# Kernel optimization log

Hardware: AMD Instinct MI355X
Metric: run time of the kernel (lower is better)

Reference implementation:

```python
import jax, jax.numpy as jnp
import numpy as np

HID = 64   # RNN_HID_SIZE
FEAT = 9   # feature dim, hard-coded in module
T = 36     # SEQ_LEN


def setup_inputs() -> dict:
    key = jax.random.key(0)
    ks = jax.random.split(key, 20)
    B = 16384

    def u(k, shape, stdv):
        return jax.random.uniform(k, shape, jnp.float32, -stdv, stdv)

    s_h = 1.0 / np.sqrt(HID)    # stdv for layers with 64 rows / fan-in 64
    s_f = 1.0 / np.sqrt(FEAT)   # stdv 1/3 for feature-sized layers
    s_c = 1.0 / np.sqrt(2 * FEAT)  # weight_combine: Linear(18, 9)

    inp = {
        "values": jax.random.normal(ks[0], (B, T, FEAT), jnp.float32),
        "masks": (jax.random.uniform(ks[1], (B, T, FEAT)) < 0.8).astype(jnp.float32),
        "deltas": jax.random.uniform(ks[2], (B, T, FEAT), jnp.float32, 0.0, 5.0),
        # TemporalDecay h: W [64, 9], stdv = 1/sqrt(64)
        "W_gh": u(ks[3], (HID, FEAT), s_h), "b_gh": u(ks[4], (HID,), s_h),
        # TemporalDecay x (diag): W [9, 9], stdv = 1/sqrt(9)
        "W_gx": u(ks[5], (FEAT, FEAT), s_f), "b_gx": u(ks[6], (FEAT,), s_f),
        # hist_reg: Linear(64, 9)
        "W_hist": u(ks[7], (FEAT, HID), s_h), "b_hist": u(ks[8], (FEAT,), s_h),
        "W_feat": u(ks[9], (FEAT, FEAT), s_f), "b_feat": u(ks[10], (FEAT,), s_f),
        # weight_combine: Linear(18, 9)
        "W_comb": u(ks[11], (FEAT, 2 * FEAT), s_c), "b_comb": u(ks[12], (FEAT,), s_c),
        # LSTMCell(18, 64): gates order i, f, g, o
        "W_ih": u(ks[13], (4 * HID, 2 * FEAT), s_h), "W_hh": u(ks[14], (4 * HID, HID), s_h),
        "b_ih": u(ks[15], (4 * HID,), s_h), "b_hh": u(ks[16], (4 * HID,), s_h),
    }
    return inp


def reference(values, masks, deltas, W_gh, b_gh, W_gx, b_gx, W_hist, b_hist,
              W_feat, b_feat, W_comb, b_comb, W_ih, W_hh, b_ih, b_hh):
    B = values.shape[0]
    dt = values.dtype
    eye = jnp.eye(FEAT, dtype=dt)
    Wgx_diag = W_gx * eye            # TemporalDecay diag mask
    Wfeat_off = W_feat * (1.0 - eye)

    # time-major for scan: [T, B, F]
    xs = (jnp.swapaxes(values, 0, 1), jnp.swapaxes(masks, 0, 1), jnp.swapaxes(deltas, 0, 1))

    def step(carry, xt):
        h, c, loss = carry
        x, m, d = xt
        gamma_h = jnp.exp(-jax.nn.relu(d @ W_gh.T + b_gh))   # [B, 64]
        gamma_x = jnp.exp(-jax.nn.relu(d @ Wgx_diag.T + b_gx))  # [B, 9]
        h = h * gamma_h
        x_h = h @ W_hist.T + b_hist
        denom = jnp.sum(m) + 1e-5
        x_c = m * x + (1.0 - m) * x_h
        z_h = x_c @ Wfeat_off.T + b_feat
        alpha = jnp.concatenate([gamma_x, m], axis=1) @ W_comb.T + b_comb
        c_h = alpha * z_h + (1.0 - alpha) * x_h
        loss = loss + (jnp.sum(jnp.abs(x - x_h) * m)
                       + jnp.sum(jnp.abs(x - z_h) * m)
                       + jnp.sum(jnp.abs(x - c_h) * m)) / denom
        c_c = m * x + (1.0 - m) * c_h
        inp = jnp.concatenate([c_c, m], axis=1)              # [B, 18]
        gates = inp @ W_ih.T + b_ih + h @ W_hh.T + b_hh      # [B, 256]
        i, f, g, o = jnp.split(gates, 4, axis=1)
        c = jax.nn.sigmoid(f) * c + jax.nn.sigmoid(i) * jnp.tanh(g)
        h = jax.nn.sigmoid(o) * jnp.tanh(c)
        return (h, c, loss), c_c

    init = (jnp.zeros((B, HID), dt), jnp.zeros((B, HID), dt), jnp.zeros((), dt))
    (_, _, loss), imps = jax.lax.scan(step, init, xs)
    imputations = jnp.swapaxes(imps, 0, 1)  # [B, T, F]
    return loss / T, imputations
```

## Files before the change

### kernel.cpp

```cpp
#include <hip/hip_runtime.h>

typedef _Float16 hh;
typedef _Float16 h2  __attribute__((ext_vector_type(2)));
typedef _Float16 v4h __attribute__((ext_vector_type(4)));
typedef _Float16 v8h __attribute__((ext_vector_type(8)));
typedef float v4f    __attribute__((ext_vector_type(4)));
typedef unsigned short u16;

#define T_STEPS 36
#define FEAT 9
#define HID 64
#define BT 32
#define SIN_STR 264
#define PK_STR 40

__device__ __forceinline__ float fast_exp2(float x) {
#if __has_builtin(__builtin_amdgcn_exp2f)
  return __builtin_amdgcn_exp2f(x);
#else
  return exp2f(x);
#endif
}
__device__ __forceinline__ float fast_rcp(float x) {
#if __has_builtin(__builtin_amdgcn_rcpf)
  return __builtin_amdgcn_rcpf(x);
#else
  return 1.f / x;
#endif
}
__device__ __forceinline__ float sigmoid_fast(float x) {
  return fast_rcp(1.f + fast_exp2(x * -1.442695041f));
}
__device__ __forceinline__ float tanh_fast(float x) {
  return 1.f - 2.f * fast_rcp(1.f + fast_exp2(x * 2.885390082f));
}
__device__ __forceinline__ float fdot2(h2 a, h2 b, float c) {
#if __has_builtin(__builtin_amdgcn_fdot2)
  return __builtin_amdgcn_fdot2(a, b, c, false);
#else
  return c + (float)a[0] * (float)b[0] + (float)a[1] * (float)b[1];
#endif
}
__device__ __forceinline__ h2 mkh2(hh a, hh b) { h2 r; r[0] = a; r[1] = b; return r; }
__device__ __forceinline__ v4f mfma16(v8h a, v8h b, v4f c) {
  return __builtin_amdgcn_mfma_f32_16x16x32_f16(a, b, c, 0, 0, 0);
}

__global__ void zero_ws(float* __restrict__ ws, float* __restrict__ out) {
  int tid = threadIdx.x;
  if (tid < T_STEPS) ws[tid] = 0.f;
  if (tid == 0) out[0] = 0.f;
}

__global__ __launch_bounds__(256) void denom_kernel(const float* __restrict__ masks,
                                                    float* __restrict__ ws) {
  __shared__ float red[T_STEPS];
  const int tid = threadIdx.x;
  if (tid < T_STEPS) red[tid] = 0.f;
  __syncthreads();
  const int idx = blockIdx.x * 256 + tid;
  const int t0 = (idx % 9) * 4;
  const float4* p = (const float4*)masks + (size_t)idx * 9;
  float acc[4] = {0.f, 0.f, 0.f, 0.f};
#pragma unroll
  for (int c = 0; c < 9; ++c) {
    float4 v = p[c];
    acc[(4 * c) / 9]     += v.x;
    acc[(4 * c + 1) / 9] += v.y;
    acc[(4 * c + 2) / 9] += v.z;
    acc[(4 * c + 3) / 9] += v.w;
  }
#pragma unroll
  for (int j = 0; j < 4; ++j) atomicAdd(&red[t0 + j], acc[j]);
  __syncthreads();
  if (tid < T_STEPS) atomicAdd(&ws[tid], red[tid]);
}

__global__ __launch_bounds__(256) void denom_part(const float* __restrict__ masks,
                                                  float* __restrict__ ws) {
  __shared__ float red[T_STEPS];
  const int tid = threadIdx.x;
  if (tid < T_STEPS) red[tid] = 0.f;
  __syncthreads();
  const int idx = blockIdx.x * 256 + tid;
  const int t0 = (idx % 9) * 4;
  const float4* p = (const float4*)masks + (size_t)idx * 9;
  float acc[4] = {0.f, 0.f, 0.f, 0.f};
#pragma unroll
  for (int c = 0; c < 9; ++c) {
    float4 v = p[c];
    acc[(4 * c) / 9]     += v.x;
    acc[(4 * c + 1) / 9] += v.y;
    acc[(4 * c + 2) / 9] += v.z;
    acc[(4 * c + 3) / 9] += v.w;
  }
#pragma unroll
  for (int j = 0; j < 4; ++j) atomicAdd(&red[t0 + j], acc[j]);
  __syncthreads();
  if (tid < T_STEPS) ws[64 + blockIdx.x * T_STEPS + tid] = red[tid];
}

__global__ __launch_bounds__(576) void denom_final(float* __restrict__ ws,
                                                   float* __restrict__ out,
                                                   int nblocks) {
  __shared__ float red[576];
  const int tid = threadIdx.x;
  const int t = tid >> 4;
  const int l = tid & 15;
  float s = 0.f;
  for (int b = l; b < nblocks; b += 16) s += ws[64 + b * T_STEPS + t];
  red[tid] = s;
  __syncthreads();
  if (l < 8) red[tid] += red[tid + 8];
  __syncthreads();
  if (l < 4) red[tid] += red[tid + 4];
  __syncthreads();
  if (l < 2) red[tid] += red[tid + 2];
  __syncthreads();
  if (l == 0) ws[t] = red[tid] + red[tid + 1];
  if (tid == 0) out[0] = 0.f;
}

#define BARX() asm volatile("s_waitcnt lgkmcnt(0)\n\ts_barrier" ::: "memory")

#define RITS_STEP(t, pxC,pmC,pdC,pxCb,pmCb,pdCb, pxN,pmN,pdN,pxNb,pmNb,pdNb)   \
  {                                                                            \
    const float inv_den = fast_rcp(denom[(t)] + 1e-5f);                        \
    const int pb = ((t) & 1) * 96;                                             \
         \
    v4f gacc[2];                                                               \
    {                                                                          \
      const int sel = ((t) + 1) & 1;                                           \
      const int awin = 176 + sel * 24;                                         \
      _Pragma("unroll")                                                        \
      for (int mt = 0; mt < 2; ++mt) {                                         \
        v8h a_ = *(const v8h*)&sIn[(mt * 16 + nlo) * SIN_STR + awin + q * 8];  \
        v4f z4 = {0.f, 0.f, 0.f, 0.f};                                         \
        gacc[mt] = sel ? mfma16(a_, bGamB, z4) : mfma16(a_, bGamA, z4);        \
      }                                                                        \
    }                                                                          \
         \
    {                                                                          \
      v8h a_ = *(const v8h*)&sIn[(mtw * 16 + nlo) * SIN_STR + 232 + q * 8];    \
      v4f z4 = {0.f, 0.f, 0.f, 0.f};                                           \
      v4f aacc = mfma16(a_, bAl, z4);                                          \
      if ((q >> 1) == (wid & 1) && nlo < 9) {                                  \
        _Pragma("unroll")                                                      \
        for (int r = 0; r < 4; ++r)                                            \
          sPk[(mtw * 16 + q * 4 + r) * PK_STR + 27 + nlo] = (hh)aacc[r];       \
      }                                                                        \
    }                                                                          \
       \
    {                                                                          \
      v4f xacc = {0.f, 0.f, 0.f, 0.f};                                         \
      _Pragma("unroll")                                                        \
      for (int kt = 0; kt < 3; ++kt) {                                         \
        v8h a_ = *(const v8h*)&sIn[(mtw * 16 + nlo) * SIN_STR + pb +           \
                                   kt * 32 + q * 8];                           \
        xacc = mfma16(a_, bH[kt], xacc);                                       \
      }                                                                        \
      if ((q >> 1) == (wid & 1) && nlo < 9) {                                  \
        _Pragma("unroll")                                                      \
        for (int r = 0; r < 4; ++r)                                            \
          sPk[(mtw * 16 + q * 4 + r) * PK_STR + 18 + nlo] = (hh)xacc[r];       \
      }                                                                        \
    }                                                                          \
           \
    asm volatile("s_waitcnt lgkmcnt(0)" ::: "memory");                         \
         \
    {                                                                          \
      const int pk = eP * PK_STR;                                              \
      float x_f  = (float)sPk[pk + fqw];                                       \
      float m_f  = (float)sPk[pk + 9 + fqw];                                   \
      float xh_f = (float)sPk[pk + 18 + fqw];                                  \
      float a1   = (float)sPk[pk + 27 + fqw];                                  \
      v8h r0 = *(const v8h*)&sPk[pk];                                          \
      v8h r1 = *(const v8h*)&sPk[pk + 8];                                      \
      v8h r2 = *(const v8h*)&sPk[pk + 16];                                     \
      v8h r3 = *(const v8h*)&sPk[pk + 24];                                     \
      hh xxh[9] = {r0[0],r0[1],r0[2],r0[3],r0[4],r0[5],r0[6],r0[7],r1[0]};     \
      hh mmh[9] = {r1[1],r1[2],r1[3],r1[4],r1[5],r1[6],r1[7],r2[0],r2[1]};     \
      hh xhh[9] = {r2[2],r2[3],r2[4],r2[5],r2[6],r2[7],r3[0],r3[1],r3[2]};     \
      hh xch[10];                                                              \
      _Pragma("unroll")                                                        \
      for (int f = 0; f < 9; ++f) {                                            \
        u16 mb = __builtin_bit_cast(u16, mmh[f]);                              \
        xch[f] = mb ? xxh[f] : xhh[f];                                         \
      }                                                                        \
      xch[9] = (hh)0.f;                                                        \
      h2 xc2[5] = {mkh2(xch[0],xch[1]), mkh2(xch[2],xch[3]),                   \
                   mkh2(xch[4],xch[5]), mkh2(xch[6],xch[7]),                   \
                   mkh2(xch[8],xch[9])};                                       \
      float z1a = bf1, z1b = 0.f;                                              \
      z1a = fdot2(wf1[0], xc2[0], z1a); z1b = fdot2(wf1[1], xc2[1], z1b);      \
      z1a = fdot2(wf1[2], xc2[2], z1a); z1b = fdot2(wf1[3], xc2[3], z1b);      \
      z1a = fdot2(wf1[4], xc2[4], z1a);                                        \
      float z1 = z1a + z1b;                                                    \
      float ch1 = xh_f + a1 * (z1 - xh_f);                                     \
      bool obs1 = (m_f != 0.f);                                                \
      float cc1 = obs1 ? x_f : ch1;                                            \
      float lterm = obs1 ? (fabsf(x_f - xh_f) + fabsf(x_f - z1) +              \
                            fabsf(x_f - ch1)) : 0.f;                           \
      sIn[eP * SIN_STR + pb + fqw] = (hh)cc1;                                  \
      sIn[eP * SIN_STR + pb + 9 + fqw] = (hh)m_f;                              \
      op1[0] = cc1;                                                            \
      if (fqw == 7) {                                                          \
        float a2 = (float)sPk[pk + 27 + 8];                                    \
        float z2a = bf2, z2b = 0.f;                                            \
        z2a = fdot2(wf2[0], xc2[0], z2a); z2b = fdot2(wf2[1], xc2[1], z2b);    \
        z2a = fdot2(wf2[2], xc2[2], z2a); z2b = fdot2(wf2[3], xc2[3], z2b);    \
        z2a = fdot2(wf2[4], xc2[4], z2a);                                      \
        float z2 = z2a + z2b;                                                  \
        float x8 = (float)xxh[8], m8 = (float)mmh[8], xh8 = (float)xhh[8];     \
        float ch2 = xh8 + a2 * (z2 - xh8);                                     \
        bool obs2 = (m8 != 0.f);                                               \
        float cc2 = obs2 ? x8 : ch2;                                           \
        lterm += obs2 ? (fabsf(x8 - xh8) + fabsf(x8 - z2) +                    \
                         fabsf(x8 - ch2)) : 0.f;                               \
        sIn[eP * SIN_STR + pb + 8] = (hh)cc2;                                  \
        sIn[eP * SIN_STR + pb + 17] = mmh[8];                                  \
        op1[1] = cc2;                                                          \
      }                                                                        \
      loss_acc += lterm * inv_den;                                             \
      op1 += FEAT;                                                             \
    }                                                                          \
    BARX();                                                                    \
      \
    {                                                                          \
      const bool ldN = ((t) + 2 < T_STEPS);                                    \
      const bool ldD = ((t) + 3 < T_STEPS);                                    \
      if (ldN) {                                                               \
        size_t offn = (size_t)(b0 + e1) * (T_STEPS * FEAT) +                   \
                      ((t) + 2) * FEAT + f1;                                   \
        pxN = values[offn]; pmN = masks[offn];                                 \
        if (tid < 32) {                                                        \
          size_t offn2 = (size_t)(b0 + e2g) * (T_STEPS * FEAT) +               \
                         ((t) + 2) * FEAT + f2g;                               \
          pxNb = values[offn2]; pmNb = masks[offn2];                           \
        }                                                                      \
      }                                                                        \
      if (ldD) {                                                               \
        size_t offd = (size_t)(b0 + e1) * (T_STEPS * FEAT) +                   \
                      ((t) + 3) * FEAT + f1;                                   \
        pdN = deltas[offd];                                                    \
        if (tid < 32) {                                                        \
          size_t offd2 = (size_t)(b0 + e2g) * (T_STEPS * FEAT) +               \
                         ((t) + 3) * FEAT + f2g;                               \
          pdNb = deltas[offd2];                                                \
        }                                                                      \
      }                                                                        \
      const int pub = (((t) + 1) & 1) * 96;                                    \
      v8h af[2][3];                                                            \
      _Pragma("unroll")                                                        \
      for (int mt = 0; mt < 2; ++mt)                                           \
        _Pragma("unroll")                                                      \
        for (int kt = 0; kt < 3; ++kt)                                         \
          af[mt][kt] = *(const v8h*)&sIn[(mt * 16 + nlo) * SIN_STR + pb +      \
                                         kt * 32 + q * 8];                     \
      v4f acc[2][4];                                                           \
      _Pragma("unroll")                                                        \
      for (int mt = 0; mt < 2; ++mt)                                           \
        _Pragma("unroll")                                                      \
        for (int p = 0; p < 4; ++p)                                            \
          acc[mt][p] = (v4f){0.f, 0.f, 0.f, 0.f};                              \
      _Pragma("unroll")                                                        \
      for (int mt = 0; mt < 2; ++mt)                                           \
        _Pragma("unroll")                                                      \
        for (int p = 0; p < 4; ++p)                                            \
          _Pragma("unroll")                                                    \
          for (int kt = 0; kt < 3; ++kt)                                       \
            acc[mt][p] = mfma16(af[mt][kt], bG[p][kt], acc[mt][p]);            \
      _Pragma("unroll")                                                        \
      for (int mt = 0; mt < 2; ++mt) {                                         \
        _Pragma("unroll")                                                      \
        for (int r = 0; r < 4; ++r) {                                          \
          float ig = sigmoid_fast(acc[mt][0][r]);                              \
          float fg = sigmoid_fast(acc[mt][1][r]);                              \
          float gg = tanh_fast(acc[mt][2][r]);                                 \
          float og = sigmoid_fast(acc[mt][3][r]);                              \
          float cn = fg * c_s[mt * 4 + r] + ig * gg;                           \
          c_s[mt * 4 + r] = cn;                                                \
          float hn = og * tanh_fast(cn);                                       \
          float gam = fast_exp2(fmaxf(gacc[mt][r], 0.f) * -1.442695041f);      \
          sIn[(mt * 16 + q * 4 + r) * SIN_STR + pub + 18 + j_col] =            \
              (hh)(hn * gam);                                                  \
        }                                                                      \
      }                                                                        \
      if ((t) + 1 < T_STEPS) {                                                 \
        sPk[e1 * PK_STR + f1] = (hh)pxC;                                       \
        sPk[e1 * PK_STR + 9 + f1] = (hh)pmC;                                   \
        sIn[e1 * SIN_STR + 233 + f1] =                                         \
            (hh)fast_exp2(fmaxf(dH * wgx1 + bgx1, 0.f) * -1.442695041f);       \
        sIn[e1 * SIN_STR + 242 + f1] = (hh)pmC;                                \
        if (tid < 32) {                                                        \
          sPk[e2g * PK_STR + f2g] = (hh)pxCb;                                  \
          sPk[e2g * PK_STR + 9 + f2g] = (hh)pmCb;                              \
          sIn[e2g * SIN_STR + 233 + f2g] =                                     \
              (hh)fast_exp2(fmaxf(dHb * wgx2 + bgx2, 0.f) * -1.442695041f);    \
          sIn[e2g * SIN_STR + 242 + f2g] = (hh)pmCb;                           \
        }                                                                      \
      }                                                                        \
      if ((t) + 2 < T_STEPS) {                                                 \
        const int sb = 192 + ((t) & 1) * 10;                                   \
        sIn[e1 * SIN_STR + sb + f1] = (hh)pdC;                                 \
        if (tid < 32) sIn[e2g * SIN_STR + sb + f2g] = (hh)pdCb;                \
      }                                                                        \
      dH = pdC; dHb = pdCb;                                                    \
    }                                                                          \
    BARX();                                                                    \
  }

__global__ __launch_bounds__(256, 2) void rits_kernel(
    const float* __restrict__ values, const float* __restrict__ masks,
    const float* __restrict__ deltas,
    const float* __restrict__ W_gh, const float* __restrict__ b_gh,
    const float* __restrict__ W_gx, const float* __restrict__ b_gx,
    const float* __restrict__ W_hist, const float* __restrict__ b_hist,
    const float* __restrict__ W_feat, const float* __restrict__ b_feat,
    const float* __restrict__ W_comb, const float* __restrict__ b_comb,
    const float* __restrict__ W_ih, const float* __restrict__ W_hh,
    const float* __restrict__ b_ih, const float* __restrict__ b_hh,
    const float* __restrict__ denom, float* __restrict__ out) {

  __shared__ __align__(16) hh sIn[BT * SIN_STR];
  __shared__ __align__(16) hh sPk[BT * PK_STR];
  __shared__ float sRed[256];

  const int tid = threadIdx.x;
  const int lane = tid & 63;
  const int wid = tid >> 6;
  const int q = lane >> 4;
  const int nlo = lane & 15;
  const int b0 = blockIdx.x * BT;
  const int j_col = 16 * wid + nlo;
  const int mtw = wid >> 1;

  v8h bG[4][3];
#pragma unroll
  for (int p = 0; p < 4; ++p)
#pragma unroll
    for (int kt = 0; kt < 3; ++kt) {
      int n = 64 * p + j_col;
      v8h r;
#pragma unroll
      for (int jj = 0; jj < 8; ++jj) {
        int k = kt * 32 + q * 8 + jj;
        float v = 0.f;
        if (k < 18)       v = W_ih[n * 18 + k];
        else if (k < 82)  v = W_hh[n * 64 + (k - 18)];
        else if (k == 82) v = b_ih[n] + b_hh[n];
        r[jj] = (hh)v;
      }
      bG[p][kt] = r;
    }
  v8h bH[3];
#pragma unroll
  for (int kt = 0; kt < 3; ++kt) {
    v8h r;
#pragma unroll
    for (int jj = 0; jj < 8; ++jj) {
      int k = kt * 32 + q * 8 + jj;
      float v = 0.f;
      if (nlo < 9) {
        if (k >= 18 && k < 82) v = W_hist[nlo * 64 + (k - 18)];
        else if (k == 82)      v = b_hist[nlo];
      }
      r[jj] = (hh)v;
    }
    bH[kt] = r;
  }
  v8h bGamA, bGamB;
  {
    int n = j_col;
    v8h ra, rb;
#pragma unroll
    for (int jj = 0; jj < 8; ++jj) {
      int k = q * 8 + jj;
      float va = 0.f, vb = 0.f;
      if (k == 2) va = b_gh[n];
      else if (k >= 16 && k < 25) va = W_gh[n * 9 + (k - 16)];
      if (k >= 2 && k < 11) vb = W_gh[n * 9 + (k - 2)];
      else if (k == 12) vb = b_gh[n];
      ra[jj] = (hh)va; rb[jj] = (hh)vb;
    }
    bGamA = ra; bGamB = rb;
  }
  v8h bAl;
  {
    v8h r;
#pragma unroll
    for (int jj = 0; jj < 8; ++jj) {
      int k = q * 8 + jj;
      float v = 0.f;
      if (nlo < 9) {
        if (k == 0)       v = b_comb[nlo];
        else if (k < 10)  v = W_comb[nlo * 18 + (k - 1)];
        else if (k < 19)  v = W_comb[nlo * 18 + 9 + (k - 10)];
      }
      r[jj] = (hh)v;
    }
    bAl = r;
  }

  const int eP = tid >> 3, fqw = tid & 7;
  h2 wf1[5], wf2[5];
  float bf1 = b_feat[fqw], bf2 = b_feat[8];
#pragma unroll
  for (int j = 0; j < 5; ++j) {
    int i0 = 2 * j, i1 = 2 * j + 1;
    hh a0 = (hh)((i0 == fqw) ? 0.f : W_feat[fqw * 9 + i0]);
    hh a1 = (hh)((i1 < 9) ? ((i1 == fqw) ? 0.f : W_feat[fqw * 9 + i1]) : 0.f);
    wf1[j] = mkh2(a0, a1);
    hh c0 = (hh)((i0 == 8) ? 0.f : W_feat[8 * 9 + i0]);
    hh c1 = (hh)((i1 < 9) ? W_feat[8 * 9 + i1] : 0.f);
    wf2[j] = mkh2(c0, c1);
  }

  const int e1 = tid / 9, f1 = tid - 9 * e1;
  const int e2g = (tid + 256) / 9, f2g = (tid + 256) - 9 * e2g;
  const float wgx1 = W_gx[f1 * 9 + f1], bgx1 = b_gx[f1];
  float wgx2 = 0.f, bgx2 = 0.f;
  if (tid < 32) { wgx2 = W_gx[f2g * 9 + f2g]; bgx2 = b_gx[f2g]; }

  float* op1 = out + 1 + (size_t)(b0 + eP) * (T_STEPS * FEAT) + fqw;

  for (int i = tid; i < BT * SIN_STR; i += 256) sIn[i] = (hh)0.f;
  __syncthreads();
  if (tid < BT) {
    sIn[tid * SIN_STR + 82] = (hh)1.f;
    sIn[tid * SIN_STR + 178] = (hh)1.f;
    sIn[tid * SIN_STR + 212] = (hh)1.f;
    sIn[tid * SIN_STR + 232] = (hh)1.f;
  }
  float pA_x = 0.f, pA_m = 0.f, pA_d = 0.f, pA_xb = 0.f, pA_mb = 0.f, pA_db = 0.f;
  float pB_x = 0.f, pB_m = 0.f, pB_d = 0.f, pB_xb = 0.f, pB_mb = 0.f, pB_db = 0.f;
  float dH = 0.f, dHb = 0.f;
  {
    size_t off = (size_t)(b0 + e1) * (T_STEPS * FEAT) + f1;
    float d0 = deltas[off];
    float m0 = masks[off];
    sPk[e1 * PK_STR + f1] = (hh)values[off];
    sPk[e1 * PK_STR + 9 + f1] = (hh)m0;
    sIn[e1 * SIN_STR + 233 + f1] =
        (hh)fast_exp2(fmaxf(d0 * wgx1 + bgx1, 0.f) * -1.442695041f);
    sIn[e1 * SIN_STR + 242 + f1] = (hh)m0;
    float d1 = deltas[off + FEAT];
    dH = d1;
    sIn[e1 * SIN_STR + 202 + f1] = (hh)d1;
    pA_x = values[off + FEAT]; pA_m = masks[off + FEAT];
    pA_d = deltas[off + 2 * FEAT];
    if (tid < 32) {
      size_t off2 = (size_t)(b0 + e2g) * (T_STEPS * FEAT) + f2g;
      float d0b = deltas[off2];
      float m0b = masks[off2];
      sPk[e2g * PK_STR + f2g] = (hh)values[off2];
      sPk[e2g * PK_STR + 9 + f2g] = (hh)m0b;
      sIn[e2g * SIN_STR + 233 + f2g] =
          (hh)fast_exp2(fmaxf(d0b * wgx2 + bgx2, 0.f) * -1.442695041f);
      sIn[e2g * SIN_STR + 242 + f2g] = (hh)m0b;
      float d1b = deltas[off2 + FEAT];
      dHb = d1b;
      sIn[e2g * SIN_STR + 202 + f2g] = (hh)d1b;
      pA_xb = values[off2 + FEAT]; pA_mb = masks[off2 + FEAT];
      pA_db = deltas[off2 + 2 * FEAT];
    }
  }
  __syncthreads();

  float c_s[8];
#pragma unroll
  for (int i = 0; i < 8; ++i) c_s[i] = 0.f;
  float loss_acc = 0.f;

  for (int t = 0; t < T_STEPS; t += 2) {
    RITS_STEP(t,     pA_x, pA_m, pA_d, pA_xb, pA_mb, pA_db,
                     pB_x, pB_m, pB_d, pB_xb, pB_mb, pB_db);
    RITS_STEP(t + 1, pB_x, pB_m, pB_d, pB_xb, pB_mb, pB_db,
                     pA_x, pA_m, pA_d, pA_xb, pA_mb, pA_db);
  }

  sRed[tid] = loss_acc;
  __syncthreads();
  for (int k = 128; k > 0; k >>= 1) {
    if (tid < k) sRed[tid] += sRed[tid + k];
    __syncthreads();
  }
  if (tid == 0) atomicAdd(out, sRed[0] * (1.f / (float)T_STEPS));
}

extern "C" void kernel_launch(void* const* d_in, const int* in_sizes, int n_in,
                              void* d_out, int out_size, void* d_ws, size_t ws_size,
                              hipStream_t stream) {
  const float* values = (const float*)d_in[0];
  const float* masks  = (const float*)d_in[1];
  const float* deltas = (const float*)d_in[2];
  const float* W_gh   = (const float*)d_in[3];
  const float* b_gh   = (const float*)d_in[4];
  const float* W_gx   = (const float*)d_in[5];
  const float* b_gx   = (const float*)d_in[6];
  const float* W_hist = (const float*)d_in[7];
  const float* b_hist = (const float*)d_in[8];
  const float* W_feat = (const float*)d_in[9];
  const float* b_feat = (const float*)d_in[10];
  const float* W_comb = (const float*)d_in[11];
  const float* b_comb = (const float*)d_in[12];
  const float* W_ih   = (const float*)d_in[13];
  const float* W_hh   = (const float*)d_in[14];
  const float* b_ih   = (const float*)d_in[15];
  const float* b_hh   = (const float*)d_in[16];

  float* out = (float*)d_out;
  float* ws  = (float*)d_ws;
  int B = in_sizes[0] / (T_STEPS * FEAT);
  int nb1 = (B * 9) / 256;

  size_t need = (size_t)(64 + (size_t)nb1 * T_STEPS) * sizeof(float);
  if (ws_size >= need) {
    denom_part<<<nb1, 256, 0, stream>>>(masks, ws);
    denom_final<<<1, 576, 0, stream>>>(ws, out, nb1);
  } else {
    zero_ws<<<1, 64, 0, stream>>>(ws, out);
    denom_kernel<<<nb1, 256, 0, stream>>>(masks, ws);
  }
  rits_kernel<<<B / BT, 256, 0, stream>>>(values, masks, deltas,
                                          W_gh, b_gh, W_gx, b_gx,
                                          W_hist, b_hist, W_feat, b_feat,
                                          W_comb, b_comb, W_ih, W_hh,
                                          b_ih, b_hh, ws, out);
}
```

Baseline: 245.3 us.

## Precompute h-dependent LSTM gate MFMAs before the barrier to shorten the critical path

The gate matmul is split by K-tile. The two K-tiles that depend only on the decayed hidden state (kt=1,2) are now issued early, before the elementwise imputation phase and its barrier. Only the kt=0 tile, which depends on the freshly written c_c/m inputs, stays after the barrier. The history-regression MFMA is also reordered to go first. This is meant to overlap MFMA latency with the scalar imputation work, at the cost of holding 8 extra accumulator vectors in registers across the phase.

```diff
diff --git a/kernel.cpp b/kernel.cpp
--- a/kernel.cpp
+++ b/kernel.cpp
@@ -127,16 +127,21 @@
   {                                                                            \
     const float inv_den = fast_rcp(denom[(t)] + 1e-5f);                        \
     const int pb = ((t) & 1) * 96;                                             \
-         \
     v4f gacc[2];                                                               \
+    v4f gAcc[2][4];       \
+       \
     {                                                                          \
-      const int sel = ((t) + 1) & 1;                                           \
-      const int awin = 176 + sel * 24;                                         \
-      _Pragma("unroll")                                                        \
-      for (int mt = 0; mt < 2; ++mt) {                                         \
-        v8h a_ = *(const v8h*)&sIn[(mt * 16 + nlo) * SIN_STR + awin + q * 8];  \
-        v4f z4 = {0.f, 0.f, 0.f, 0.f};                                         \
-        gacc[mt] = sel ? mfma16(a_, bGamB, z4) : mfma16(a_, bGamA, z4);        \
+      v4f xacc = {0.f, 0.f, 0.f, 0.f};                                         \
+      _Pragma("unroll")                                                        \
+      for (int kt = 0; kt < 3; ++kt) {                                         \
+        v8h a_ = *(const v8h*)&sIn[(mtw * 16 + nlo) * SIN_STR + pb +           \
+                                   kt * 32 + q * 8];                           \
+        xacc = mfma16(a_, bH[kt], xacc);                                       \
+      }                                                                        \
+      if ((q >> 1) == (wid & 1) && nlo < 9) {                                  \
+        _Pragma("unroll")                                                      \
+        for (int r = 0; r < 4; ++r)                                            \
+          sPk[(mtw * 16 + q * 4 + r) * PK_STR + 18 + nlo] = (hh)xacc[r];       \
       }                                                                        \
     }                                                                          \
          \
@@ -150,19 +155,28 @@
           sPk[(mtw * 16 + q * 4 + r) * PK_STR + 27 + nlo] = (hh)aacc[r];       \
       }                                                                        \
     }                                                                          \
-       \
+         \
     {                                                                          \
-      v4f xacc = {0.f, 0.f, 0.f, 0.f};                                         \
-      _Pragma("unroll")                                                        \
-      for (int kt = 0; kt < 3; ++kt) {                                         \
-        v8h a_ = *(const v8h*)&sIn[(mtw * 16 + nlo) * SIN_STR + pb +           \
-                                   kt * 32 + q * 8];                           \
-        xacc = mfma16(a_, bH[kt], xacc);                                       \
-      }                                                                        \
-      if ((q >> 1) == (wid & 1) && nlo < 9) {                                  \
+      const int sel = ((t) + 1) & 1;                                           \
+      const int awin = 176 + sel * 24;                                         \
+      _Pragma("unroll")                                                        \
+      for (int mt = 0; mt < 2; ++mt) {                                         \
+        v8h a_ = *(const v8h*)&sIn[(mt * 16 + nlo) * SIN_STR + awin + q * 8];  \
+        v4f z4 = {0.f, 0.f, 0.f, 0.f};                                         \
+        gacc[mt] = sel ? mfma16(a_, bGamB, z4) : mfma16(a_, bGamA, z4);        \
+      }                                                                        \
+    }                                                                          \
+     \
+    {                                                                          \
+      _Pragma("unroll")                                                        \
+      for (int mt = 0; mt < 2; ++mt) {                                         \
+        v8h a1 = *(const v8h*)&sIn[(mt * 16 + nlo) * SIN_STR + pb + 32 + q * 8]; \
+        v8h a2 = *(const v8h*)&sIn[(mt * 16 + nlo) * SIN_STR + pb + 64 + q * 8]; \
         _Pragma("unroll")                                                      \
-        for (int r = 0; r < 4; ++r)                                            \
-          sPk[(mtw * 16 + q * 4 + r) * PK_STR + 18 + nlo] = (hh)xacc[r];       \
+        for (int p = 0; p < 4; ++p) {                                          \
+          v4f z4 = {0.f, 0.f, 0.f, 0.f};                                       \
+          gAcc[mt][p] = mfma16(a2, bG[p][2], mfma16(a1, bG[p][1], z4));        \
+        }                                                                      \
       }                                                                        \
     }                                                                          \
            \
@@ -225,7 +239,7 @@
       op1 += FEAT;                                                             \
     }                                                                          \
     BARX();                                                                    \
-      \
+       \
     {                                                                          \
       const bool ldN = ((t) + 2 < T_STEPS);                                    \
       const bool ldD = ((t) + 3 < T_STEPS);                                    \
@@ -250,34 +264,23 @@
         }                                                                      \
       }                                                                        \
       const int pub = (((t) + 1) & 1) * 96;                                    \
-      v8h af[2][3];                                                            \
+      v8h af0[2];                                                              \
       _Pragma("unroll")                                                        \
       for (int mt = 0; mt < 2; ++mt)                                           \
-        _Pragma("unroll")                                                      \
-        for (int kt = 0; kt < 3; ++kt)                                         \
-          af[mt][kt] = *(const v8h*)&sIn[(mt * 16 + nlo) * SIN_STR + pb +      \
-                                         kt * 32 + q * 8];                     \
-      v4f acc[2][4];                                                           \
+        af0[mt] = *(const v8h*)&sIn[(mt * 16 + nlo) * SIN_STR + pb + q * 8];   \
       _Pragma("unroll")                                                        \
       for (int mt = 0; mt < 2; ++mt)                                           \
         _Pragma("unroll")                                                      \
         for (int p = 0; p < 4; ++p)                                            \
-          acc[mt][p] = (v4f){0.f, 0.f, 0.f, 0.f};                              \
-      _Pragma("unroll")                                                        \
-      for (int mt = 0; mt < 2; ++mt)                                           \
-        _Pragma("unroll")                                                      \
-        for (int p = 0; p < 4; ++p)                                            \
-          _Pragma("unroll")                                                    \
-          for (int kt = 0; kt < 3; ++kt)                                       \
-            acc[mt][p] = mfma16(af[mt][kt], bG[p][kt], acc[mt][p]);            \
+          gAcc[mt][p] = mfma16(af0[mt], bG[p][0], gAcc[mt][p]);                \
       _Pragma("unroll")                                                        \
       for (int mt = 0; mt < 2; ++mt) {                                         \
         _Pragma("unroll")                                                      \
         for (int r = 0; r < 4; ++r) {                                          \
-          float ig = sigmoid_fast(acc[mt][0][r]);                              \
-          float fg = sigmoid_fast(acc[mt][1][r]);                              \
-          float gg = tanh_fast(acc[mt][2][r]);                                 \
-          float og = sigmoid_fast(acc[mt][3][r]);                              \
+          float ig = sigmoid_fast(gAcc[mt][0][r]);                             \
+          float fg = sigmoid_fast(gAcc[mt][1][r]);                             \
+          float gg = tanh_fast(gAcc[mt][2][r]);                                \
+          float og = sigmoid_fast(gAcc[mt][3][r]);                             \
           float cn = fg * c_s[mt * 4 + r] + ig * gg;                           \
           c_s[mt * 4 + r] = cn;                                                \
           float hn = og * tanh_fast(cn);                                       \
```

New measurement: 246.9 us. No clear change (+0.7%).
